# Performance work log

Measured on AMD Instinct MI355X. Metric: run time of the kernel, lower is better.

Reference implementation:

```python
import jax, jax.numpy as jnp
from jax import lax
import numpy as np

HIDDEN = 32


def setup_inputs() -> dict:
    key = jax.random.key(0)
    ks = jax.random.split(key, 7)
    B, T = 4096, 512
    s = 1.0 / np.sqrt(HIDDEN)  # PyTorch default uniform init bound
    x = jax.random.normal(ks[0], (B, T), dtype=jnp.float32)
    W_ih = jax.random.uniform(ks[1], (4 * HIDDEN, 1), jnp.float32, -s, s)
    W_hh = jax.random.uniform(ks[2], (4 * HIDDEN, HIDDEN), jnp.float32, -s, s)
    b_ih = jax.random.uniform(ks[3], (4 * HIDDEN,), jnp.float32, -s, s)
    b_hh = jax.random.uniform(ks[4], (4 * HIDDEN,), jnp.float32, -s, s)
    W_fc = jax.random.uniform(ks[5], (1, HIDDEN), jnp.float32, -s, s)
    b_fc = jax.random.uniform(ks[6], (1,), jnp.float32, -s, s)
    return {"x": x, "W_ih": W_ih, "W_hh": W_hh, "b_ih": b_ih,
            "b_hh": b_hh, "W_fc": W_fc, "b_fc": b_fc}


def reference(x, W_ih, W_hh, b_ih, b_hh, W_fc, b_fc):
    B, T = x.shape
    H = HIDDEN
    # input projection is time-parallel: precompute x_t * W_ih + biases -> [T, B, 4H]
    x_proj = x.T[:, :, None] * W_ih[:, 0][None, None, :] + (b_ih + b_hh)

    def step(carry, xp):
        h, c = carry
        gates = xp + h @ W_hh.T                      # [B, 4H]
        i, f, g, o = jnp.split(gates, 4, axis=-1)    # PyTorch gate order i,f,g,o
        i = jax.nn.sigmoid(i)
        f = jax.nn.sigmoid(f)
        g = jnp.tanh(g)
        o = jax.nn.sigmoid(o)
        c = f * c + i * g
        h = o * jnp.tanh(c)
        return (h, c), None

    h0 = jnp.zeros((B, H), x.dtype)
    c0 = jnp.zeros((B, H), x.dtype)
    (h_last, _), _ = lax.scan(step, (h0, c0), x_proj)
    return h_last @ W_fc.T + b_fc                    # [B, 1]
```

## Files before the change

### kernel.cpp

```cpp
#include <hip/hip_runtime.h>


static constexpr int T_LEN = 512;
static constexpr int H = 32;

typedef _Float16 h2   __attribute__((ext_vector_type(2)));
typedef __fp16   fp2  __attribute__((ext_vector_type(2)));
typedef _Float16 v8h  __attribute__((ext_vector_type(8)));
typedef float    v4f  __attribute__((ext_vector_type(4)));

__device__ __forceinline__ v4f MF32(v8h a, v8h b, v4f c) {
#if __has_builtin(__builtin_amdgcn_mfma_f32_16x16x32_f16)
    return __builtin_amdgcn_mfma_f32_16x16x32_f16(a, b, c, 0, 0, 0);
#else
    v4f d = c;
    asm("v_mfma_f32_16x16x32_f16 %0, %1, %2, %0" : "+v"(d) : "v"(a), "v"(b));
    return d;
#endif
}

__device__ __forceinline__ v8h mkB(uint4 w) {
    union { uint4 u; v8h v; } u;
    u.u = w; return u.v;
}

__global__ void
__attribute__((amdgpu_flat_work_group_size(128, 128), amdgpu_waves_per_eu(1, 1)))
reslstm_kernel(const float* __restrict__ x,
               const float* __restrict__ W_ih,
               const float* __restrict__ W_hh,
               const float* __restrict__ b_ih,
               const float* __restrict__ b_hh,
               const float* __restrict__ W_fc,
               const float* __restrict__ b_fc,
               float* __restrict__ out, int B)
{
    __shared__ float xl[16][36];
    __shared__ uint2 hx[2][4][16][2];
    __shared__ float osum[2][16];

    const int tid  = threadIdx.x;
    const int lane = tid & 63;
    const int wv   = tid >> 6;
    const int c    = lane & 15;
    const int q    = lane >> 4;

    const int wbase = blockIdx.x << 4;
    if (wbase >= B) return;
    const int bb = wbase + c;

    constexpr float NL2E  = -1.4426950408889634f;
    constexpr float N2L2E = 2.0f * NL2E;

    v8h A8[4];
    v4f wih[4], bsb[4];
    #pragma unroll
    for (int k = 0; k < 4; ++k) {
        const int   t  = 2 * k + wv;
        const float sc = (k == 2) ? N2L2E : NL2E;
        const float4 w1 = *reinterpret_cast<const float4*>(
            W_hh + (16 * t + c) * H + 4 * q);
        const float4 w2 = *reinterpret_cast<const float4*>(
            W_hh + (16 * t + c) * H + 16 + 4 * q);
        A8[k][0] = (_Float16)(w1.x * sc); A8[k][1] = (_Float16)(w1.y * sc);
        A8[k][2] = (_Float16)(w1.z * sc); A8[k][3] = (_Float16)(w1.w * sc);
        A8[k][4] = (_Float16)(w2.x * sc); A8[k][5] = (_Float16)(w2.y * sc);
        A8[k][6] = (_Float16)(w2.z * sc); A8[k][7] = (_Float16)(w2.w * sc);
        const int r0 = 16 * t + 4 * q;
        const float4 wi = *reinterpret_cast<const float4*>(W_ih + r0);
        const float4 bi = *reinterpret_cast<const float4*>(b_ih + r0);
        const float4 bh = *reinterpret_cast<const float4*>(b_hh + r0);
        wih[k][0] = wi.x * sc; wih[k][1] = wi.y * sc;
        wih[k][2] = wi.z * sc; wih[k][3] = wi.w * sc;
        bsb[k][0] = (bi.x + bh.x) * sc; bsb[k][1] = (bi.y + bh.y) * sc;
        bsb[k][2] = (bi.z + bh.z) * sc; bsb[k][3] = (bi.w + bh.w) * sc;
    }

    float cs0 = 0.f, cs1 = 0.f, cs2 = 0.f, cs3 = 0.f;
    float hv0 = 0.f, hv1 = 0.f, hv2 = 0.f, hv3 = 0.f;
    v8h B8 = mkB(uint4{0u, 0u, 0u, 0u});

#define PINALL()                                                              \
    asm volatile("" : "+v"(A8[0]), "+v"(A8[1]), "+v"(A8[2]), "+v"(A8[3]));    \
    asm volatile("" : "+v"(wih[0]), "+v"(wih[1]), "+v"(wih[2]), "+v"(wih[3]), \
                      "+v"(bsb[0]), "+v"(bsb[1]), "+v"(bsb[2]), "+v"(bsb[3]))

#define GSTATE(AI, AF, AG, AO, CC, HH) do {                                   \
    const float Ei = __builtin_amdgcn_exp2f(AI);                              \
    const float Ef = __builtin_amdgcn_exp2f(AF);                              \
    const float Eg = __builtin_amdgcn_exp2f(AG);                              \
    const float Eo = __builtin_amdgcn_exp2f(AO);                              \
    const float Di = 1.0f + Ei, Df = 1.0f + Ef;                               \
    const float Dg = 1.0f + Eg, Do_ = 1.0f + Eo;                              \
    const float P  = Di * Dg;                                                 \
    const float t_ = (1.0f - Eg) * Df;                                        \
    const float u_ = __builtin_fmaf(CC, P, t_);                               \
    const float Rc = __builtin_amdgcn_rcpf(Df * P);                           \
    CC = u_ * Rc;                                                             \
    const float Ec = __builtin_amdgcn_exp2f(CC * N2L2E);                      \
    const float Dc = 1.0f + Ec;                                               \
    const float Rh = __builtin_amdgcn_rcpf(Do_ * Dc);                         \
    HH = (1.0f - Ec) * Rh;                                                    \
} while (0)

#define STEP(XT, PAR) do {                                                    \
    const float xt = (XT);                                                    \
    v4f acc[4];                                                               \
    _Pragma("unroll")                                                         \
    for (int k = 0; k < 4; ++k) acc[k] = bsb[k] + wih[k] * xt;                \
    _Pragma("unroll")                                                         \
    for (int k = 0; k < 4; ++k) acc[k] = MF32(A8[k], B8, acc[k]);             \
    unsigned int* slot =                                                      \
        reinterpret_cast<unsigned int*>(&hx[PAR][q][c][wv]);                  \
    GSTATE(acc[0][0], acc[1][0], acc[2][0], acc[3][0], cs0, hv0);             \
    GSTATE(acc[0][1], acc[1][1], acc[2][1], acc[3][1], cs1, hv1);             \
    slot[0] = __builtin_bit_cast(unsigned int,                                \
                  __builtin_amdgcn_cvt_pkrtz(hv0, hv1));                      \
    GSTATE(acc[0][2], acc[1][2], acc[2][2], acc[3][2], cs2, hv2);             \
    GSTATE(acc[0][3], acc[1][3], acc[2][3], acc[3][3], cs3, hv3);             \
    slot[1] = __builtin_bit_cast(unsigned int,                                \
                  __builtin_amdgcn_cvt_pkrtz(hv2, hv3));                      \
    asm volatile("s_waitcnt lgkmcnt(0)\n\ts_barrier" ::: "memory");           \
    B8 = mkB(*reinterpret_cast<const uint4*>(&hx[PAR][q][c][0]));             \
} while (0)

    const int r    = tid >> 3;
    const int colb = (tid & 7) << 2;
    const float* xsrc = x + (size_t)(wbase + r) * T_LEN + colb;
    float4 xA = *reinterpret_cast<const float4*>(xsrc);

    for (int tc = 0; tc < T_LEN / 32; ++tc) {
        PINALL();
        *reinterpret_cast<float4*>(&xl[r][colb]) = xA;
        __syncthreads();
        if (tc + 1 < T_LEN / 32)
            xA = *reinterpret_cast<const float4*>(xsrc + (tc + 1) * 32);
        const float4* xq4c = reinterpret_cast<const float4*>(&xl[c][0]);
        #pragma unroll 2
        for (int t4 = 0; t4 < 8; ++t4) {
            const float4 xv = xq4c[t4];
            STEP(xv.x, 0);
            STEP(xv.y, 1);
            STEP(xv.z, 0);
            STEP(xv.w, 1);
        }
    }
#undef STEP
#undef GSTATE
#undef PINALL

    const int u0 = 16 * wv + 4 * q;
    float val = hv0 * W_fc[u0]     + hv1 * W_fc[u0 + 1]
              + hv2 * W_fc[u0 + 2] + hv3 * W_fc[u0 + 3];
    val += __shfl_xor(val, 16);
    val += __shfl_xor(val, 32);
    if (q == 0) osum[wv][c] = val;
    __syncthreads();
    if (wv == 0 && q == 0 && bb < B)
        out[bb] = osum[0][c] + osum[1][c] + b_fc[0];
}

extern "C" void kernel_launch(void* const* d_in, const int* in_sizes, int n_in,
                              void* d_out, int out_size, void* d_ws, size_t ws_size,
                              hipStream_t stream) {
    const float* x    = (const float*)d_in[0];
    const float* W_ih = (const float*)d_in[1];
    const float* W_hh = (const float*)d_in[2];
    const float* b_ih = (const float*)d_in[3];
    const float* b_hh = (const float*)d_in[4];
    const float* W_fc = (const float*)d_in[5];
    const float* b_fc = (const float*)d_in[6];
    float* out = (float*)d_out;
    const int B = in_sizes[0] / T_LEN;
    dim3 block(128);
    dim3 grid((B + 15) / 16);
    reslstm_kernel<<<grid, block, 0, stream>>>(x, W_ih, W_hh, b_ih, b_hh,
                                               W_fc, b_fc, out, B);
}
```

Baseline: 239.9 us.

## Interleave two independent batch groups per block to hide recurrence latency

Each block now handles 32 batch rows as two 16-row groups whose LSTM steps are interleaved and share one barrier per timestep. The goal is to fill MFMA and transcendental latency bubbles in the serial recurrence with independent work, and to amortise barrier cost. In exchange the grid is halved, so fewer blocks are available to spread across compute units, and register pressure rises.

```diff
diff --git a/kernel.cpp b/kernel.cpp
--- a/kernel.cpp
+++ b/kernel.cpp
@@ -35,9 +35,9 @@
                const float* __restrict__ b_fc,
                float* __restrict__ out, int B)
 {
-    __shared__ float xl[16][36];
-    __shared__ uint2 hx[2][4][16][2];
-    __shared__ float osum[2][16];
+    __shared__ float xl[32][36];
+    __shared__ uint2 hx[2][2][4][16][2];
+    __shared__ float osum[2][2][16];
 
     const int tid  = threadIdx.x;
     const int lane = tid & 63;
@@ -45,9 +45,10 @@
     const int c    = lane & 15;
     const int q    = lane >> 4;
 
-    const int wbase = blockIdx.x << 4;
+    const int wbase = blockIdx.x << 5;
     if (wbase >= B) return;
-    const int bb = wbase + c;
+    const int bbA = wbase + c;
+    const int bbB = wbase + 16 + c;
 
     constexpr float NL2E  = -1.4426950408889634f;
     constexpr float N2L2E = 2.0f * NL2E;
@@ -76,9 +77,12 @@
         bsb[k][2] = (bi.z + bh.z) * sc; bsb[k][3] = (bi.w + bh.w) * sc;
     }
 
-    float cs0 = 0.f, cs1 = 0.f, cs2 = 0.f, cs3 = 0.f;
-    float hv0 = 0.f, hv1 = 0.f, hv2 = 0.f, hv3 = 0.f;
-    v8h B8 = mkB(uint4{0u, 0u, 0u, 0u});
+    float cA0 = 0.f, cA1 = 0.f, cA2 = 0.f, cA3 = 0.f;
+    float hA0 = 0.f, hA1 = 0.f, hA2 = 0.f, hA3 = 0.f;
+    float cB0 = 0.f, cB1 = 0.f, cB2 = 0.f, cB3 = 0.f;
+    float hB0 = 0.f, hB1 = 0.f, hB2 = 0.f, hB3 = 0.f;
+    v8h B8A = mkB(uint4{0u, 0u, 0u, 0u});
+    v8h B8B = B8A;
 
 #define PINALL()                                                              \
     asm volatile("" : "+v"(A8[0]), "+v"(A8[1]), "+v"(A8[2]), "+v"(A8[3]));    \
@@ -103,61 +107,78 @@
     HH = (1.0f - Ec) * Rh;                                                    \
 } while (0)
 
-#define STEP(XT, PAR) do {                                                    \
+#define STEPG(XT, PAR, GRP, B8R, C0, C1, C2, C3, H0, H1, H2, H3) do {         \
     const float xt = (XT);                                                    \
     v4f acc[4];                                                               \
     _Pragma("unroll")                                                         \
     for (int k = 0; k < 4; ++k) acc[k] = bsb[k] + wih[k] * xt;                \
     _Pragma("unroll")                                                         \
-    for (int k = 0; k < 4; ++k) acc[k] = MF32(A8[k], B8, acc[k]);             \
+    for (int k = 0; k < 4; ++k) acc[k] = MF32(A8[k], B8R, acc[k]);            \
     unsigned int* slot =                                                      \
-        reinterpret_cast<unsigned int*>(&hx[PAR][q][c][wv]);                  \
-    GSTATE(acc[0][0], acc[1][0], acc[2][0], acc[3][0], cs0, hv0);             \
-    GSTATE(acc[0][1], acc[1][1], acc[2][1], acc[3][1], cs1, hv1);             \
+        reinterpret_cast<unsigned int*>(&hx[GRP][PAR][q][c][wv]);             \
+    GSTATE(acc[0][0], acc[1][0], acc[2][0], acc[3][0], C0, H0);               \
+    GSTATE(acc[0][1], acc[1][1], acc[2][1], acc[3][1], C1, H1);               \
     slot[0] = __builtin_bit_cast(unsigned int,                                \
-                  __builtin_amdgcn_cvt_pkrtz(hv0, hv1));                      \
-    GSTATE(acc[0][2], acc[1][2], acc[2][2], acc[3][2], cs2, hv2);             \
-    GSTATE(acc[0][3], acc[1][3], acc[2][3], acc[3][3], cs3, hv3);             \
+                  __builtin_amdgcn_cvt_pkrtz(H0, H1));                        \
+    GSTATE(acc[0][2], acc[1][2], acc[2][2], acc[3][2], C2, H2);               \
+    GSTATE(acc[0][3], acc[1][3], acc[2][3], acc[3][3], C3, H3);               \
     slot[1] = __builtin_bit_cast(unsigned int,                                \
-                  __builtin_amdgcn_cvt_pkrtz(hv2, hv3));                      \
+                  __builtin_amdgcn_cvt_pkrtz(H2, H3));                        \
+} while (0)
+
+#define STEP2(XTA, XTB, PAR) do {                                             \
+    STEPG(XTA, PAR, 0, B8A, cA0, cA1, cA2, cA3, hA0, hA1, hA2, hA3);          \
+    STEPG(XTB, PAR, 1, B8B, cB0, cB1, cB2, cB3, hB0, hB1, hB2, hB3);          \
     asm volatile("s_waitcnt lgkmcnt(0)\n\ts_barrier" ::: "memory");           \
-    B8 = mkB(*reinterpret_cast<const uint4*>(&hx[PAR][q][c][0]));             \
+    B8A = mkB(*reinterpret_cast<const uint4*>(&hx[0][PAR][q][c][0]));         \
+    B8B = mkB(*reinterpret_cast<const uint4*>(&hx[1][PAR][q][c][0]));         \
 } while (0)
 
     const int r    = tid >> 3;
     const int colb = (tid & 7) << 2;
-    const float* xsrc = x + (size_t)(wbase + r) * T_LEN + colb;
-    float4 xA = *reinterpret_cast<const float4*>(xsrc);
+    const float* xsrcA = x + (size_t)(wbase + r) * T_LEN + colb;
+    const float* xsrcB = x + (size_t)(wbase + 16 + r) * T_LEN + colb;
+    float4 xpA = *reinterpret_cast<const float4*>(xsrcA);
+    float4 xpB = *reinterpret_cast<const float4*>(xsrcB);
 
     for (int tc = 0; tc < T_LEN / 32; ++tc) {
         PINALL();
-        *reinterpret_cast<float4*>(&xl[r][colb]) = xA;
+        *reinterpret_cast<float4*>(&xl[r][colb])      = xpA;
+        *reinterpret_cast<float4*>(&xl[16 + r][colb]) = xpB;
         __syncthreads();
-        if (tc + 1 < T_LEN / 32)
-            xA = *reinterpret_cast<const float4*>(xsrc + (tc + 1) * 32);
-        const float4* xq4c = reinterpret_cast<const float4*>(&xl[c][0]);
-        #pragma unroll 2
+        if (tc + 1 < T_LEN / 32) {
+            xpA = *reinterpret_cast<const float4*>(xsrcA + (tc + 1) * 32);
+            xpB = *reinterpret_cast<const float4*>(xsrcB + (tc + 1) * 32);
+        }
+        const float4* xqA = reinterpret_cast<const float4*>(&xl[c][0]);
+        const float4* xqB = reinterpret_cast<const float4*>(&xl[16 + c][0]);
         for (int t4 = 0; t4 < 8; ++t4) {
-            const float4 xv = xq4c[t4];
-            STEP(xv.x, 0);
-            STEP(xv.y, 1);
-            STEP(xv.z, 0);
-            STEP(xv.w, 1);
+            const float4 xvA = xqA[t4];
+            const float4 xvB = xqB[t4];
+            STEP2(xvA.x, xvB.x, 0);
+            STEP2(xvA.y, xvB.y, 1);
+            STEP2(xvA.z, xvB.z, 0);
+            STEP2(xvA.w, xvB.w, 1);
         }
     }
-#undef STEP
+#undef STEP2
+#undef STEPG
 #undef GSTATE
 #undef PINALL
 
     const int u0 = 16 * wv + 4 * q;
-    float val = hv0 * W_fc[u0]     + hv1 * W_fc[u0 + 1]
-              + hv2 * W_fc[u0 + 2] + hv3 * W_fc[u0 + 3];
-    val += __shfl_xor(val, 16);
-    val += __shfl_xor(val, 32);
-    if (q == 0) osum[wv][c] = val;
+    const float w0 = W_fc[u0],     w1 = W_fc[u0 + 1];
+    const float w2 = W_fc[u0 + 2], w3 = W_fc[u0 + 3];
+    float vA = hA0 * w0 + hA1 * w1 + hA2 * w2 + hA3 * w3;
+    float vB = hB0 * w0 + hB1 * w1 + hB2 * w2 + hB3 * w3;
+    vA += __shfl_xor(vA, 16); vA += __shfl_xor(vA, 32);
+    vB += __shfl_xor(vB, 16); vB += __shfl_xor(vB, 32);
+    if (q == 0) { osum[0][wv][c] = vA; osum[1][wv][c] = vB; }
     __syncthreads();
-    if (wv == 0 && q == 0 && bb < B)
-        out[bb] = osum[0][c] + osum[1][c] + b_fc[0];
+    if (wv == 0 && q == 0) {
+        if (bbA < B) out[bbA] = osum[0][0][c] + osum[0][1][c] + b_fc[0];
+        if (bbB < B) out[bbB] = osum[1][0][c] + osum[1][1][c] + b_fc[0];
+    }
 }
 
 extern "C" void kernel_launch(void* const* d_in, const int* in_sizes, int n_in,
@@ -173,7 +194,7 @@
     float* out = (float*)d_out;
     const int B = in_sizes[0] / T_LEN;
     dim3 block(128);
-    dim3 grid((B + 15) / 16);
+    dim3 grid((B + 31) / 32);
     reslstm_kernel<<<grid, block, 0, stream>>>(x, W_ih, W_hh, b_ih, b_hh,
                                                W_fc, b_fc, out, B);
 }
```

New measurement: 387.6 us. 61.6% more time.

## Split LSTM hidden units across four waves per 16-sequence block

Applied to the files above, without the earlier changes.

Each block of 16 sequences now runs on four waves instead of two, and each wave owns 8 hidden units instead of 16. Per step a wave issues two MFMAs instead of four and evaluates two gate-state updates per lane instead of four. Cross-lane shuffles gather the i/f/g/o pre-activations into the same lane. This shortens the serial per-step critical path, which dominates the 512-step recurrence, at the cost of extra shuffles, a four-wave barrier each step, and twice as many waves resident per CU.

```diff
diff --git a/kernel.cpp b/kernel.cpp
--- a/kernel.cpp
+++ b/kernel.cpp
@@ -25,7 +25,7 @@
 }
 
 __global__ void
-__attribute__((amdgpu_flat_work_group_size(128, 128), amdgpu_waves_per_eu(1, 1)))
+__attribute__((amdgpu_flat_work_group_size(256, 256), amdgpu_waves_per_eu(1, 1)))
 reslstm_kernel(const float* __restrict__ x,
                const float* __restrict__ W_ih,
                const float* __restrict__ W_hh,
@@ -36,14 +36,15 @@
                float* __restrict__ out, int B)
 {
     __shared__ float xl[16][36];
-    __shared__ uint2 hx[2][4][16][2];
-    __shared__ float osum[2][16];
+    __shared__ unsigned int hxu[2][16][20];
+    __shared__ float osum[4][16];
 
     const int tid  = threadIdx.x;
     const int lane = tid & 63;
     const int wv   = tid >> 6;
     const int c    = lane & 15;
     const int q    = lane >> 4;
+    const bool hiq = (lane & 32) != 0;
 
     const int wbase = blockIdx.x << 4;
     if (wbase >= B) return;
@@ -52,38 +53,51 @@
     constexpr float NL2E  = -1.4426950408889634f;
     constexpr float N2L2E = 2.0f * NL2E;
 
-    v8h A8[4];
-    v4f wih[4], bsb[4];
-    #pragma unroll
-    for (int k = 0; k < 4; ++k) {
-        const int   t  = 2 * k + wv;
-        const float sc = (k == 2) ? N2L2E : NL2E;
-        const float4 w1 = *reinterpret_cast<const float4*>(
-            W_hh + (16 * t + c) * H + 4 * q);
-        const float4 w2 = *reinterpret_cast<const float4*>(
-            W_hh + (16 * t + c) * H + 16 + 4 * q);
-        A8[k][0] = (_Float16)(w1.x * sc); A8[k][1] = (_Float16)(w1.y * sc);
-        A8[k][2] = (_Float16)(w1.z * sc); A8[k][3] = (_Float16)(w1.w * sc);
-        A8[k][4] = (_Float16)(w2.x * sc); A8[k][5] = (_Float16)(w2.y * sc);
-        A8[k][6] = (_Float16)(w2.z * sc); A8[k][7] = (_Float16)(w2.w * sc);
-        const int r0 = 16 * t + 4 * q;
-        const float4 wi = *reinterpret_cast<const float4*>(W_ih + r0);
-        const float4 bi = *reinterpret_cast<const float4*>(b_ih + r0);
-        const float4 bh = *reinterpret_cast<const float4*>(b_hh + r0);
-        wih[k][0] = wi.x * sc; wih[k][1] = wi.y * sc;
-        wih[k][2] = wi.z * sc; wih[k][3] = wi.w * sc;
-        bsb[k][0] = (bi.x + bh.x) * sc; bsb[k][1] = (bi.y + bh.y) * sc;
-        bsb[k][2] = (bi.z + bh.z) * sc; bsb[k][3] = (bi.w + bh.w) * sc;
+    const int grow0 = (c < 8) ? (8 * wv + c) : (32 + 8 * wv + c - 8);
+    const int grow1 = (c < 8) ? (64 + 8 * wv + c) : (96 + 8 * wv + c - 8);
+    const float s0 = NL2E;
+    const float s1 = (c < 8) ? N2L2E : NL2E;
+
+    v8h A80, A81;
+    {
+        const float4 w1 = *reinterpret_cast<const float4*>(W_hh + grow0 * H + 4 * q);
+        const float4 w2 = *reinterpret_cast<const float4*>(W_hh + grow0 * H + 16 + 4 * q);
+        A80[0] = (_Float16)(w1.x * s0); A80[1] = (_Float16)(w1.y * s0);
+        A80[2] = (_Float16)(w1.z * s0); A80[3] = (_Float16)(w1.w * s0);
+        A80[4] = (_Float16)(w2.x * s0); A80[5] = (_Float16)(w2.y * s0);
+        A80[6] = (_Float16)(w2.z * s0); A80[7] = (_Float16)(w2.w * s0);
+        const float4 w3 = *reinterpret_cast<const float4*>(W_hh + grow1 * H + 4 * q);
+        const float4 w4 = *reinterpret_cast<const float4*>(W_hh + grow1 * H + 16 + 4 * q);
+        A81[0] = (_Float16)(w3.x * s1); A81[1] = (_Float16)(w3.y * s1);
+        A81[2] = (_Float16)(w3.z * s1); A81[3] = (_Float16)(w3.w * s1);
+        A81[4] = (_Float16)(w4.x * s1); A81[5] = (_Float16)(w4.y * s1);
+        A81[6] = (_Float16)(w4.z * s1); A81[7] = (_Float16)(w4.w * s1);
     }
 
-    float cs0 = 0.f, cs1 = 0.f, cs2 = 0.f, cs3 = 0.f;
-    float hv0 = 0.f, hv1 = 0.f, hv2 = 0.f, hv3 = 0.f;
+    v4f wih0, bsb0, wih1, bsb1;
+    #pragma unroll
+    for (int m = 0; m < 4; ++m) {
+        const int rr = 4 * q + m;
+        const int r0 = (rr < 8) ? (8 * wv + rr) : (32 + 8 * wv + rr - 8);
+        const int r1 = (rr < 8) ? (64 + 8 * wv + rr) : (96 + 8 * wv + rr - 8);
+        const float sc1 = (rr < 8) ? N2L2E : NL2E;
+        wih0[m] = W_ih[r0] * NL2E;
+        bsb0[m] = (b_ih[r0] + b_hh[r0]) * NL2E;
+        wih1[m] = W_ih[r1] * sc1;
+        bsb1[m] = (b_ih[r1] + b_hh[r1]) * sc1;
+    }
+
+    const int u0 = 8 * wv + ((q & 1) << 2) + ((q >> 1) << 1);
+    const int p  = u0 >> 1;
+    const int slot = (p < 8) ? (((p >> 1) << 2) | (p & 1))
+                             : ((((p - 8) >> 1) << 2) | 2 | (p & 1));
+
+    float csa = 0.f, csb = 0.f, hva = 0.f, hvb = 0.f;
     v8h B8 = mkB(uint4{0u, 0u, 0u, 0u});
 
 #define PINALL()                                                              \
-    asm volatile("" : "+v"(A8[0]), "+v"(A8[1]), "+v"(A8[2]), "+v"(A8[3]));    \
-    asm volatile("" : "+v"(wih[0]), "+v"(wih[1]), "+v"(wih[2]), "+v"(wih[3]), \
-                      "+v"(bsb[0]), "+v"(bsb[1]), "+v"(bsb[2]), "+v"(bsb[3]))
+    asm volatile("" : "+v"(A80), "+v"(A81));                                  \
+    asm volatile("" : "+v"(wih0), "+v"(wih1), "+v"(bsb0), "+v"(bsb1))
 
 #define GSTATE(AI, AF, AG, AO, CC, HH) do {                                   \
     const float Ei = __builtin_amdgcn_exp2f(AI);                              \
@@ -105,35 +119,42 @@
 
 #define STEP(XT, PAR) do {                                                    \
     const float xt = (XT);                                                    \
-    v4f acc[4];                                                               \
-    _Pragma("unroll")                                                         \
-    for (int k = 0; k < 4; ++k) acc[k] = bsb[k] + wih[k] * xt;                \
-    _Pragma("unroll")                                                         \
-    for (int k = 0; k < 4; ++k) acc[k] = MF32(A8[k], B8, acc[k]);             \
-    unsigned int* slot =                                                      \
-        reinterpret_cast<unsigned int*>(&hx[PAR][q][c][wv]);                  \
-    GSTATE(acc[0][0], acc[1][0], acc[2][0], acc[3][0], cs0, hv0);             \
-    GSTATE(acc[0][1], acc[1][1], acc[2][1], acc[3][1], cs1, hv1);             \
-    slot[0] = __builtin_bit_cast(unsigned int,                                \
-                  __builtin_amdgcn_cvt_pkrtz(hv0, hv1));                      \
-    GSTATE(acc[0][2], acc[1][2], acc[2][2], acc[3][2], cs2, hv2);             \
-    GSTATE(acc[0][3], acc[1][3], acc[2][3], acc[3][3], cs3, hv3);             \
-    slot[1] = __builtin_bit_cast(unsigned int,                                \
-                  __builtin_amdgcn_cvt_pkrtz(hv2, hv3));                      \
+    v4f a0 = bsb0 + wih0 * xt;                                                \
+    v4f a1 = bsb1 + wih1 * xt;                                                \
+    a0 = MF32(A80, B8, a0);                                                   \
+    a1 = MF32(A81, B8, a1);                                                   \
+    const float r00 = __shfl_xor(a0[0], 32), r01 = __shfl_xor(a0[1], 32);     \
+    const float r02 = __shfl_xor(a0[2], 32), r03 = __shfl_xor(a0[3], 32);     \
+    const float r10 = __shfl_xor(a1[0], 32), r11 = __shfl_xor(a1[1], 32);     \
+    const float r12 = __shfl_xor(a1[2], 32), r13 = __shfl_xor(a1[3], 32);     \
+    const float AI0 = hiq ? r02 : a0[0];                                      \
+    const float AF0 = hiq ? a0[2] : r00;                                      \
+    const float AG0 = hiq ? r12 : a1[0];                                      \
+    const float AO0 = hiq ? a1[2] : r10;                                      \
+    const float AI1 = hiq ? r03 : a0[1];                                      \
+    const float AF1 = hiq ? a0[3] : r01;                                      \
+    const float AG1 = hiq ? r13 : a1[1];                                      \
+    const float AO1 = hiq ? a1[3] : r11;                                      \
+    GSTATE(AI0, AF0, AG0, AO0, csa, hva);                                     \
+    GSTATE(AI1, AF1, AG1, AO1, csb, hvb);                                     \
+    hxu[PAR][c][slot] = __builtin_bit_cast(unsigned int,                      \
+                            __builtin_amdgcn_cvt_pkrtz(hva, hvb));            \
     asm volatile("s_waitcnt lgkmcnt(0)\n\ts_barrier" ::: "memory");           \
-    B8 = mkB(*reinterpret_cast<const uint4*>(&hx[PAR][q][c][0]));             \
+    B8 = mkB(*reinterpret_cast<const uint4*>(&hxu[PAR][c][q << 2]));          \
 } while (0)
 
     const int r    = tid >> 3;
     const int colb = (tid & 7) << 2;
-    const float* xsrc = x + (size_t)(wbase + r) * T_LEN + colb;
-    float4 xA = *reinterpret_cast<const float4*>(xsrc);
+    const float* xsrc = x + (size_t)(wbase + (r & 15)) * T_LEN + colb;
+    float4 xA;
+    if (tid < 128) xA = *reinterpret_cast<const float4*>(xsrc);
 
     for (int tc = 0; tc < T_LEN / 32; ++tc) {
         PINALL();
-        *reinterpret_cast<float4*>(&xl[r][colb]) = xA;
+        if (tid < 128)
+            *reinterpret_cast<float4*>(&xl[r][colb]) = xA;
         __syncthreads();
-        if (tc + 1 < T_LEN / 32)
+        if (tid < 128 && tc + 1 < T_LEN / 32)
             xA = *reinterpret_cast<const float4*>(xsrc + (tc + 1) * 32);
         const float4* xq4c = reinterpret_cast<const float4*>(&xl[c][0]);
         #pragma unroll 2
@@ -149,15 +170,13 @@
 #undef GSTATE
 #undef PINALL
 
-    const int u0 = 16 * wv + 4 * q;
-    float val = hv0 * W_fc[u0]     + hv1 * W_fc[u0 + 1]
-              + hv2 * W_fc[u0 + 2] + hv3 * W_fc[u0 + 3];
+    float val = hva * W_fc[u0] + hvb * W_fc[u0 + 1];
     val += __shfl_xor(val, 16);
     val += __shfl_xor(val, 32);
     if (q == 0) osum[wv][c] = val;
     __syncthreads();
     if (wv == 0 && q == 0 && bb < B)
-        out[bb] = osum[0][c] + osum[1][c] + b_fc[0];
+        out[bb] = osum[0][c] + osum[1][c] + osum[2][c] + osum[3][c] + b_fc[0];
 }
 
 extern "C" void kernel_launch(void* const* d_in, const int* in_sizes, int n_in,
@@ -172,7 +191,7 @@
     const float* b_fc = (const float*)d_in[6];
     float* out = (float*)d_out;
     const int B = in_sizes[0] / T_LEN;
-    dim3 block(128);
+    dim3 block(256);
     dim3 grid((B + 15) / 16);
     reslstm_kernel<<<grid, block, 0, stream>>>(x, W_ih, W_hh, b_ih, b_hh,
                                                W_fc, b_fc, out, B);
```

Measured after the change: 246.4 us. +2.7%, slower.

## Split recurrent MFMA into own-half and partner-half to shorten the LDS dependency

Applied to the files above, without the earlier changes.

Each step's 16x16x32 MFMA becomes two 16x16x16 MFMAs. The first uses the wave's own freshly computed h, held in registers, so it no longer waits on shared memory. The second uses the partner wave's h, read from LDS after the barrier, and that read is moved to the start of the next step. The aim is to take the LDS round trip off the critical path and let the own-half MFMA overlap the partner read. The cost is twice as many MFMA instructions, more A-fragment registers, and a zero-initialised hx buffer.

```diff
diff --git a/kernel.cpp b/kernel.cpp
--- a/kernel.cpp
+++ b/kernel.cpp
@@ -6,21 +6,28 @@
 
 typedef _Float16 h2   __attribute__((ext_vector_type(2)));
 typedef __fp16   fp2  __attribute__((ext_vector_type(2)));
-typedef _Float16 v8h  __attribute__((ext_vector_type(8)));
+typedef _Float16 v4h  __attribute__((ext_vector_type(4)));
 typedef float    v4f  __attribute__((ext_vector_type(4)));
 
-__device__ __forceinline__ v4f MF32(v8h a, v8h b, v4f c) {
-#if __has_builtin(__builtin_amdgcn_mfma_f32_16x16x32_f16)
-    return __builtin_amdgcn_mfma_f32_16x16x32_f16(a, b, c, 0, 0, 0);
+__device__ __forceinline__ v4f MF16(v4h a, v4h b, v4f c) {
+#if __has_builtin(__builtin_amdgcn_mfma_f32_16x16x16f16)
+    return __builtin_amdgcn_mfma_f32_16x16x16f16(a, b, c, 0, 0, 0);
 #else
     v4f d = c;
-    asm("v_mfma_f32_16x16x32_f16 %0, %1, %2, %0" : "+v"(d) : "v"(a), "v"(b));
+    asm("v_mfma_f32_16x16x16_f16 %0, %1, %2, %0" : "+v"(d) : "v"(a), "v"(b));
     return d;
 #endif
 }
 
-__device__ __forceinline__ v8h mkB(uint4 w) {
-    union { uint4 u; v8h v; } u;
+__device__ __forceinline__ v4h comb4(fp2 a, fp2 b) {
+    union { h2 p[2]; v4h v; } u;
+    u.p[0] = __builtin_bit_cast(h2, a);
+    u.p[1] = __builtin_bit_cast(h2, b);
+    return u.v;
+}
+
+__device__ __forceinline__ v4h mkB4(uint2 w) {
+    union { uint2 u; v4h v; } u;
     u.u = w; return u.v;
 }
 
@@ -52,7 +59,7 @@
     constexpr float NL2E  = -1.4426950408889634f;
     constexpr float N2L2E = 2.0f * NL2E;
 
-    v8h A8[4];
+    v4h Aown[4], Apart[4];
     v4f wih[4], bsb[4];
     #pragma unroll
     for (int k = 0; k < 4; ++k) {
@@ -62,10 +69,13 @@
             W_hh + (16 * t + c) * H + 4 * q);
         const float4 w2 = *reinterpret_cast<const float4*>(
             W_hh + (16 * t + c) * H + 16 + 4 * q);
-        A8[k][0] = (_Float16)(w1.x * sc); A8[k][1] = (_Float16)(w1.y * sc);
-        A8[k][2] = (_Float16)(w1.z * sc); A8[k][3] = (_Float16)(w1.w * sc);
-        A8[k][4] = (_Float16)(w2.x * sc); A8[k][5] = (_Float16)(w2.y * sc);
-        A8[k][6] = (_Float16)(w2.z * sc); A8[k][7] = (_Float16)(w2.w * sc);
+        v4h a0, a1;
+        a0[0] = (_Float16)(w1.x * sc); a0[1] = (_Float16)(w1.y * sc);
+        a0[2] = (_Float16)(w1.z * sc); a0[3] = (_Float16)(w1.w * sc);
+        a1[0] = (_Float16)(w2.x * sc); a1[1] = (_Float16)(w2.y * sc);
+        a1[2] = (_Float16)(w2.z * sc); a1[3] = (_Float16)(w2.w * sc);
+        Aown[k]  = (wv == 0) ? a0 : a1;
+        Apart[k] = (wv == 0) ? a1 : a0;
         const int r0 = 16 * t + 4 * q;
         const float4 wi = *reinterpret_cast<const float4*>(W_ih + r0);
         const float4 bi = *reinterpret_cast<const float4*>(b_ih + r0);
@@ -78,10 +88,15 @@
 
     float cs0 = 0.f, cs1 = 0.f, cs2 = 0.f, cs3 = 0.f;
     float hv0 = 0.f, hv1 = 0.f, hv2 = 0.f, hv3 = 0.f;
-    v8h B8 = mkB(uint4{0u, 0u, 0u, 0u});
+    v4h Bown = comb4(__builtin_amdgcn_cvt_pkrtz(0.f, 0.f),
+                     __builtin_amdgcn_cvt_pkrtz(0.f, 0.f));
+
+    hx[1][q][c][wv] = uint2{0u, 0u};
 
 #define PINALL()                                                              \
-    asm volatile("" : "+v"(A8[0]), "+v"(A8[1]), "+v"(A8[2]), "+v"(A8[3]));    \
+    asm volatile("" : "+v"(Aown[0]), "+v"(Aown[1]), "+v"(Aown[2]),            \
+                      "+v"(Aown[3]), "+v"(Apart[0]), "+v"(Apart[1]),          \
+                      "+v"(Apart[2]), "+v"(Apart[3]));                        \
     asm volatile("" : "+v"(wih[0]), "+v"(wih[1]), "+v"(wih[2]), "+v"(wih[3]), \
                       "+v"(bsb[0]), "+v"(bsb[1]), "+v"(bsb[2]), "+v"(bsb[3]))
 
@@ -103,25 +118,28 @@
     HH = (1.0f - Ec) * Rh;                                                    \
 } while (0)
 
-#define STEP(XT, PAR) do {                                                    \
+#define STEP(XT, PW, PRd) do {                                                \
+    const v4h Bpart = mkB4(hx[PRd][q][c][wv ^ 1]);        \
     const float xt = (XT);                                                    \
     v4f acc[4];                                                               \
     _Pragma("unroll")                                                         \
     for (int k = 0; k < 4; ++k) acc[k] = bsb[k] + wih[k] * xt;                \
     _Pragma("unroll")                                                         \
-    for (int k = 0; k < 4; ++k) acc[k] = MF32(A8[k], B8, acc[k]);             \
+    for (int k = 0; k < 4; ++k) acc[k] = MF16(Aown[k], Bown, acc[k]);         \
+    _Pragma("unroll")                                                         \
+    for (int k = 0; k < 4; ++k) acc[k] = MF16(Apart[k], Bpart, acc[k]);       \
     unsigned int* slot =                                                      \
-        reinterpret_cast<unsigned int*>(&hx[PAR][q][c][wv]);                  \
+        reinterpret_cast<unsigned int*>(&hx[PW][q][c][wv]);                   \
     GSTATE(acc[0][0], acc[1][0], acc[2][0], acc[3][0], cs0, hv0);             \
     GSTATE(acc[0][1], acc[1][1], acc[2][1], acc[3][1], cs1, hv1);             \
-    slot[0] = __builtin_bit_cast(unsigned int,                                \
-                  __builtin_amdgcn_cvt_pkrtz(hv0, hv1));                      \
+    const fp2 pk01 = __builtin_amdgcn_cvt_pkrtz(hv0, hv1);                    \
+    slot[0] = __builtin_bit_cast(unsigned int, pk01);                         \
     GSTATE(acc[0][2], acc[1][2], acc[2][2], acc[3][2], cs2, hv2);             \
     GSTATE(acc[0][3], acc[1][3], acc[2][3], acc[3][3], cs3, hv3);             \
-    slot[1] = __builtin_bit_cast(unsigned int,                                \
-                  __builtin_amdgcn_cvt_pkrtz(hv2, hv3));                      \
+    const fp2 pk23 = __builtin_amdgcn_cvt_pkrtz(hv2, hv3);                    \
+    slot[1] = __builtin_bit_cast(unsigned int, pk23);                         \
+    Bown = comb4(pk01, pk23);                                                 \
     asm volatile("s_waitcnt lgkmcnt(0)\n\ts_barrier" ::: "memory");           \
-    B8 = mkB(*reinterpret_cast<const uint4*>(&hx[PAR][q][c][0]));             \
 } while (0)
 
     const int r    = tid >> 3;
@@ -139,10 +157,10 @@
         #pragma unroll 2
         for (int t4 = 0; t4 < 8; ++t4) {
             const float4 xv = xq4c[t4];
-            STEP(xv.x, 0);
-            STEP(xv.y, 1);
-            STEP(xv.z, 0);
-            STEP(xv.w, 1);
+            STEP(xv.x, 0, 1);
+            STEP(xv.y, 1, 0);
+            STEP(xv.z, 0, 1);
+            STEP(xv.w, 1, 0);
         }
     }
 #undef STEP
```

New measurement: 247.5 us. 1.03x slower.
